# Performance work log

Hardware: AMD Instinct MI355X
Metric: run time of the kernel (lower is better)

Reference implementation:

```python
import jax, jax.numpy as jnp
import numpy as np

SMALL = -1000.0


def setup_inputs() -> dict:
    key = jax.random.key(0)
    k1, k2, k3, k4 = jax.random.split(key, 4)
    B, T, L = 256, 1024, 64
    pred = jax.random.normal(k1, (B, T, L), dtype=jnp.float32)
    seq_len = jax.random.randint(k2, (B,), T // 2, T + 1)  # lengths in [T/2, T]
    ref = jax.random.randint(k3, (B, T), 0, L)
    # zero-pad tags beyond seq_len (required by the original end-tag indexing trick)
    ref = jnp.where(jnp.arange(T)[None, :] < seq_len[:, None], ref, 0)
    transitions = jax.random.normal(k4, (L + 2, L + 2), dtype=jnp.float32) * 0.1
    return {"pred": pred, "transitions": transitions, "ref": ref, "seq_len": seq_len}


def crf_neg_log_likelihood(pred, transitions, ref, seq_len):
    B, T, L = pred.shape
    dt = pred.dtype
    # --- build padded observations [B, T+2, L+2] ---
    obs_mid = jnp.concatenate([pred, jnp.full((B, T, 2), SMALL, dt)], axis=2)
    b_s = jnp.concatenate([jnp.full((L,), SMALL), jnp.array([0.0, SMALL])]).astype(dt)
    r_p = jnp.concatenate([jnp.zeros((L,)), jnp.array([SMALL, SMALL])]).astype(dt)
    obs = jnp.concatenate(
        [jnp.broadcast_to(b_s, (B, 1, L + 2)), obs_mid, jnp.broadcast_to(r_p, (B, 1, L + 2))],
        axis=1,
    )
    e_s = jnp.concatenate([jnp.full((L,), SMALL), jnp.array([0.0, 1000.0])]).astype(dt)
    obs = obs.at[jnp.arange(B), seq_len + 1].add(e_s)

    # --- forward algorithm: logsumexp recurrence over time ---
    def step(prev, ob):  # prev [B, L+2], ob [B, L+2]
        new = jax.nn.logsumexp(prev[:, :, None] + ob[:, None, :] + transitions[None], axis=1)
        return new, new

    prev0 = obs[:, 0]
    obs_t = jnp.swapaxes(obs[:, 1:], 0, 1)  # [T+1, B, L+2] time-major
    _, paths = jax.lax.scan(step, prev0, obs_t)  # paths [T+1, B, L+2]
    all_paths_scores = jax.nn.logsumexp(paths[seq_len, jnp.arange(B)], axis=1).sum()

    # --- gold path score ---
    mask = (jnp.arange(T)[None, :] < seq_len[:, None]).astype(dt)
    gold_emit = jnp.sum(jnp.take_along_axis(pred, ref[..., None], axis=2)[..., 0] * mask)
    padded = jnp.concatenate(
        [jnp.full((B, 1), L, ref.dtype), ref, jnp.zeros((B, 1), ref.dtype)], axis=1
    )  # [B, T+2]
    padded = padded.at[jnp.arange(B), seq_len + 1].add(L + 1)  # end tag id = L+1
    trans_sc = transitions[padded[:, :-1], padded[:, 1:]]  # [B, T+1]
    mask2 = (jnp.arange(T + 1)[None, :] < (seq_len + 1)[:, None]).astype(dt)
    gold = gold_emit + jnp.sum(trans_sc * mask2)
    return all_paths_scores - gold


def reference(pred, transitions, ref, seq_len):
    return crf_neg_log_likelihood(pred, transitions, ref, seq_len)
```

## Files before the change

### kernel.cpp

```cpp
#include <hip/hip_runtime.h>
#include <hip/hip_bf16.h>


#define RL_F(x, i) __uint_as_float(__builtin_amdgcn_readlane(__float_as_uint(x), (i)))
#define L2E 1.44269504088896340736f
#define LN2 0.69314718055994530942f

#define V_ALL(M) M(0) M(1) M(2) M(3) M(4) M(5) M(6) M(7) M(8) M(9) M(10) M(11) \
 M(12) M(13) M(14) M(15) M(16) M(17) M(18) M(19) M(20) M(21) M(22) M(23) M(24) \
 M(25) M(26) M(27) M(28) M(29) M(30) M(31) M(32) M(33) M(34) M(35) M(36) M(37) \
 M(38) M(39) M(40) M(41) M(42) M(43) M(44) M(45) M(46) M(47) M(48) M(49) M(50) \
 M(51) M(52) M(53) M(54) M(55) M(56) M(57) M(58) M(59) M(60) M(61) M(62) M(63)

#define DECLV(q) float V##q;
#define LOADF(q) V##q = __builtin_amdgcn_exp2f(tcol[(q) * 66] * L2E);
#define LOADB(q) V##q = __builtin_amdgcn_exp2f(trow[(q)] * L2E);

#define FMA4(a,b,c,d) \
    s0 = fmaf(RL_F(x,a), V##a, s0); s1 = fmaf(RL_F(x,b), V##b, s1); \
    s2 = fmaf(RL_F(x,c), V##c, s2); s3 = fmaf(RL_F(x,d), V##d, s3);
#define FMA_ALL \
    FMA4(0,1,2,3)     FMA4(4,5,6,7)     FMA4(8,9,10,11)   FMA4(12,13,14,15) \
    FMA4(16,17,18,19) FMA4(20,21,22,23) FMA4(24,25,26,27) FMA4(28,29,30,31) \
    FMA4(32,33,34,35) FMA4(36,37,38,39) FMA4(40,41,42,43) FMA4(44,45,46,47) \
    FMA4(48,49,50,51) FMA4(52,53,54,55) FMA4(56,57,58,59) FMA4(60,61,62,63)

#define ROWF(i) pb[(((i) < 0) ? 0 : (((i) > 1023) ? 1023 : (i))) * 64]

#define STEPM(p) { \
    float E = __builtin_amdgcn_exp2f((p) * L2E); \
    float x = FWD ? a : a * E; \
    float s0 = 0.f, s1 = 0.f, s2 = 0.f, s3 = 0.f; \
    FMA_ALL \
    float s = (s0 + s1) + (s2 + s3); \
    a = FWD ? s * E : s; \
    unsigned abits = (unsigned)__builtin_amdgcn_readfirstlane((int)__float_as_uint(a)); \
    int k = (int)((abits >> 23) & 255u) - 127; \
    K += k; \
    a *= __uint_as_float((unsigned)(127 - k) << 23); }

template<bool FWD>
__device__ __forceinline__ void chain(const float* __restrict__ pred,
                                      const float* __restrict__ trans,
                                      int b, int lane, int sl, int h,
                                      float* __restrict__ wsV,
                                      int* __restrict__ wsK)
{
    const float* pb   = pred + (size_t)b * 65536 + lane;
    const float* tcol = trans + lane;
    const float* trow = trans + lane * 66;
    (void)tcol; (void)trow;

    V_ALL(DECLV)
    if (FWD) { V_ALL(LOADF) } else { V_ALL(LOADB) }

    float a;
    int   K = 0;
    if (FWD) a = __builtin_amdgcn_exp2f((pb[0] + trans[64 * 66 + lane]) * L2E);
    else     a = __builtin_amdgcn_exp2f(trow[65] * L2E);

    const int dir = FWD ? 1 : -1;
    int n = FWD ? h - 1 : sl - h;
    int r = FWD ? 1 : sl - 1;

    float p0 = ROWF(r), p1 = ROWF(r + dir), p2 = ROWF(r + 2 * dir), p3 = ROWF(r + 3 * dir);
    while (n >= 4) {
        float q0 = ROWF(r + 4 * dir), q1 = ROWF(r + 5 * dir),
              q2 = ROWF(r + 6 * dir), q3 = ROWF(r + 7 * dir);
        STEPM(p0) STEPM(p1) STEPM(p2) STEPM(p3)
        p0 = q0; p1 = q1; p2 = q2; p3 = q3;
        r += 4 * dir; n -= 4;
    }
    if (n > 0) { STEPM(p0) --n; }
    if (n > 0) { STEPM(p1) --n; }
    if (n > 0) { STEPM(p2) }

    wsV[b * 64 + lane] = a;
    if (lane == 0) wsK[b] = K;
}

__global__ __launch_bounds__(64, 1) __attribute__((amdgpu_waves_per_eu(1)))
void chain_kernel(const float* __restrict__ pred,
                  const float* __restrict__ trans,
                  const int*   __restrict__ ref,
                  const int*   __restrict__ seqlen,
                  float* __restrict__ wsA, float* __restrict__ wsB,
                  int* __restrict__ wsKf, int* __restrict__ wsKb,
                  float* __restrict__ out)
{
    const int role = blockIdx.x >> 8;
    const int b    = blockIdx.x & 255;
    const int lane = threadIdx.x;
    const int sl   = seqlen[b];
    const int h    = (sl + 1) >> 1;

    if (role == 0) {
        chain<true>(pred, trans, b, lane, sl, h, wsA, wsKf);
    } else if (role == 1) {
        chain<false>(pred, trans, b, lane, sl, h, wsB, wsKb);
    } else {
        const int*   rb = ref  + b * 1024;
        const float* pg = pred + (size_t)b * 65536;
        float acc = 0.f;
        for (int t = lane; t <= sl; t += 64) {
            int from = (t == 0) ? 64 : rb[t - 1];
            int cur  = (t < sl) ? rb[t] : 65;
            acc += trans[from * 66 + cur];
            if (t < sl) acc += pg[t * 64 + cur];
        }
        #pragma unroll
        for (int off = 32; off; off >>= 1) acc += __shfl_xor(acc, off, 64);
        if (lane == 0) atomicAdd(out, -acc);
    }
}

__global__ __launch_bounds__(64) void combine_kernel(
    const float* __restrict__ wsA, const float* __restrict__ wsB,
    const int* __restrict__ wsKf, const int* __restrict__ wsKb,
    float* __restrict__ out)
{
    const int b = blockIdx.x, lane = threadIdx.x;
    float z = wsA[b * 64 + lane] * wsB[b * 64 + lane];
    #pragma unroll
    for (int off = 32; off; off >>= 1) z += __shfl_xor(z, off, 64);
    if (lane == 0) {
        float res = LN2 * (__builtin_amdgcn_logf(z) + (float)(wsKf[b] + wsKb[b]));
        atomicAdd(out, res);
    }
}

extern "C" void kernel_launch(void* const* d_in, const int* in_sizes, int n_in,
                              void* d_out, int out_size, void* d_ws, size_t ws_size,
                              hipStream_t stream) {
    const float* pred   = (const float*)d_in[0];
    const float* trans  = (const float*)d_in[1];
    const int*   ref    = (const int*)d_in[2];
    const int*   seqlen = (const int*)d_in[3];
    float* out = (float*)d_out;

    float* wsA  = (float*)d_ws;
    float* wsB  = wsA + 256 * 64;
    int*   wsKf = (int*)(wsB + 256 * 64);
    int*   wsKb = wsKf + 256;

    hipMemsetAsync(out, 0, sizeof(float), stream);
    chain_kernel<<<768, 64, 0, stream>>>(pred, trans, ref, seqlen,
                                         wsA, wsB, wsKf, wsKb, out);
    combine_kernel<<<256, 64, 0, stream>>>(wsA, wsB, wsKf, wsKb, out);
}
```

Measured before the change: 223.2 us.

## Renormalize once per four steps and precompute emission exponentials off the critical path

Moves the per-step exponent renormalization (readfirstlane plus scaling) to once every four recurrence steps, and computes exp of the prefetched emission rows one iteration ahead so the exp is off the serial dependency chain. Pins the 64 transition-exponential registers with empty asm so the compiler keeps them in VGPRs, and adjusts the launch-bound attributes. Values can grow over four unnormalized steps, which risks overflow when scores are large, though with transitions near zero and unit-normal emissions the growth should stay within float range.

```diff
diff --git a/kernel.cpp b/kernel.cpp
--- a/kernel.cpp
+++ b/kernel.cpp
@@ -15,6 +15,7 @@
 #define DECLV(q) float V##q;
 #define LOADF(q) V##q = __builtin_amdgcn_exp2f(tcol[(q) * 66] * L2E);
 #define LOADB(q) V##q = __builtin_amdgcn_exp2f(trow[(q)] * L2E);
+#define PINV(q)  asm volatile("" : "+v"(V##q));
 
 #define FMA4(a,b,c,d) \
     s0 = fmaf(RL_F(x,a), V##a, s0); s1 = fmaf(RL_F(x,b), V##b, s1); \
@@ -26,14 +27,16 @@
     FMA4(48,49,50,51) FMA4(52,53,54,55) FMA4(56,57,58,59) FMA4(60,61,62,63)
 
 #define ROWF(i) pb[(((i) < 0) ? 0 : (((i) > 1023) ? 1023 : (i))) * 64]
+#define EXPE(p) __builtin_amdgcn_exp2f((p) * L2E)
 
-#define STEPM(p) { \
-    float E = __builtin_amdgcn_exp2f((p) * L2E); \
-    float x = FWD ? a : a * E; \
+#define STEPN(E) { \
+    float x = FWD ? a : a * (E); \
     float s0 = 0.f, s1 = 0.f, s2 = 0.f, s3 = 0.f; \
     FMA_ALL \
     float s = (s0 + s1) + (s2 + s3); \
-    a = FWD ? s * E : s; \
+    a = FWD ? s * (E) : s; }
+
+#define RENORM { \
     unsigned abits = (unsigned)__builtin_amdgcn_readfirstlane((int)__float_as_uint(a)); \
     int k = (int)((abits >> 23) & 255u) - 127; \
     K += k; \
@@ -53,6 +56,7 @@
 
     V_ALL(DECLV)
     if (FWD) { V_ALL(LOADF) } else { V_ALL(LOADB) }
+    V_ALL(PINV)
 
     float a;
     int   K = 0;
@@ -63,23 +67,26 @@
     int n = FWD ? h - 1 : sl - h;
     int r = FWD ? 1 : sl - 1;
 
-    float p0 = ROWF(r), p1 = ROWF(r + dir), p2 = ROWF(r + 2 * dir), p3 = ROWF(r + 3 * dir);
+    float E0 = EXPE(ROWF(r)), E1 = EXPE(ROWF(r + dir)),
+          E2 = EXPE(ROWF(r + 2 * dir)), E3 = EXPE(ROWF(r + 3 * dir));
     while (n >= 4) {
-        float q0 = ROWF(r + 4 * dir), q1 = ROWF(r + 5 * dir),
-              q2 = ROWF(r + 6 * dir), q3 = ROWF(r + 7 * dir);
-        STEPM(p0) STEPM(p1) STEPM(p2) STEPM(p3)
-        p0 = q0; p1 = q1; p2 = q2; p3 = q3;
+        float F0 = ROWF(r + 4 * dir), F1 = ROWF(r + 5 * dir),
+              F2 = ROWF(r + 6 * dir), F3 = ROWF(r + 7 * dir);
+        STEPN(E0) STEPN(E1) STEPN(E2) STEPN(E3)
+        RENORM
+        E0 = EXPE(F0); E1 = EXPE(F1); E2 = EXPE(F2); E3 = EXPE(F3);
         r += 4 * dir; n -= 4;
     }
-    if (n > 0) { STEPM(p0) --n; }
-    if (n > 0) { STEPM(p1) --n; }
-    if (n > 0) { STEPM(p2) }
+    if (n > 0) { STEPN(E0) --n; }
+    if (n > 0) { STEPN(E1) --n; }
+    if (n > 0) { STEPN(E2) }
+    RENORM
 
     wsV[b * 64 + lane] = a;
     if (lane == 0) wsK[b] = K;
 }
 
-__global__ __launch_bounds__(64, 1) __attribute__((amdgpu_waves_per_eu(1)))
+__global__ __launch_bounds__(64) __attribute__((amdgpu_waves_per_eu(1, 1)))
 void chain_kernel(const float* __restrict__ pred,
                   const float* __restrict__ trans,
                   const int*   __restrict__ ref,
```

Result: faster. 209.5 us (-6.2%).
